# Kernel tuning notes

Measured on AMD Instinct MI355X. Metric: run time of the kernel, lower is better.

The kernel has to match this reference:

```python
import jax, jax.numpy as jnp
import numpy as np
from jax.scipy.special import logsumexp

TEMPERATURE = 0.1
EPS = 1e-8  # matches torch F.cosine_similarity eps


def setup_inputs() -> dict:
    key = jax.random.key(0)
    k1, k2 = jax.random.split(key)
    N, D, NUM_CLASSES = 8192, 256, 64
    embeddings = jax.random.normal(k1, (N, D), dtype=jnp.float32)
    target = jax.random.randint(k2, (N,), 0, NUM_CLASSES, dtype=jnp.int64)
    return {"embeddings": embeddings, "target": target}


def reference(embeddings, target):
    N = target.shape[0]
    # cosine similarity: normalize rows, then a single GEMM for all pairs
    norms = jnp.linalg.norm(embeddings, axis=-1, keepdims=True)
    e = embeddings / jnp.maximum(norms, EPS)
    sim = (e @ e.T) / TEMPERATURE  # [N, N]

    pos = target[:, None] == target[None, :]  # [N, N] bool, incl. diagonal
    diag = jnp.eye(N, dtype=bool)
    neg_inf = jnp.asarray(-jnp.inf, dtype=sim.dtype)

    # denominator: negatives only (positives masked to -inf)
    lse_neg = logsumexp(jnp.where(pos, neg_inf, sim), axis=1)
    # numerator: positives excluding self (diagonal masked to -inf)
    lse_pos = logsumexp(jnp.where(pos & ~diag, sim, neg_inf), axis=1)

    loss = lse_neg - lse_pos
    return loss.sum()
```

## Files before the change

kernel.cpp:

```cpp
#include <hip/hip_runtime.h>
#include <hip/hip_bf16.h>
#include <stdint.h>
#include <math.h>

#define NROWS 8192
#define DIM   256
#define RB    256
#define BI    128
#define JBLK  512
#define NBJS  4
#define NG    (NROWS/JBLK)
#define NIT   (NROWS/BI)

typedef __attribute__((ext_vector_type(4)))  int   int4v;
typedef __attribute__((ext_vector_type(8)))  int   int8v;
typedef __attribute__((ext_vector_type(16))) float floatx16;

typedef const __attribute__((address_space(1))) uint32_t gas_u32;
typedef __attribute__((address_space(3))) uint32_t las_u32;

#define SCALE_1_16 0x7B7B7B7B
#define L2E10      14.4269504088896f

__device__ __forceinline__ void gload_lds16(const void* g, void* l) {
    __builtin_amdgcn_global_load_lds((gas_u32*)(uintptr_t)g,
                                     (las_u32*)(uintptr_t)l, 16, 0, 0);
}

__global__ __launch_bounds__(256) void normalize_kernel(const float* __restrict__ emb,
                                                        uint32_t* __restrict__ e8,
                                                        float* __restrict__ out)
{
    if (blockIdx.x == 0 && threadIdx.x == 0) *out = 0.f;
    int row  = blockIdx.x * 4 + (threadIdx.x >> 6);
    int lane = threadIdx.x & 63;
    const float4* rowp = (const float4*)(emb + (size_t)row * DIM);
    float4 v = rowp[lane];
    float ss = v.x*v.x + v.y*v.y + v.z*v.z + v.w*v.w;
    #pragma unroll
    for (int off = 32; off > 0; off >>= 1)
        ss += __shfl_xor(ss, off, 64);
    float inv = 16.0f / fmaxf(sqrtf(ss), 1e-8f);
    int r = __builtin_amdgcn_cvt_pk_fp8_f32(v.x * inv, v.y * inv, 0, false);
    r     = __builtin_amdgcn_cvt_pk_fp8_f32(v.z * inv, v.w * inv, r, true);
    e8[(size_t)row * (DIM / 4) + lane] = (uint32_t)r;
}

template<bool DIAG>
__device__ __forceinline__ void epi(const floatx16 acc[2][2],
                                    const int* __restrict__ tgt,
                                    int jb, const int tiv[2], const int ic[2],
                                    float ps[2], float ts[2])
{
    #pragma unroll
    for (int jt = 0; jt < 2; ++jt) {
        #pragma unroll
        for (int rq = 0; rq < 4; ++rq) {
            const int jg_ = jb + jt * 32 + rq * 8;
            const int4v t4 = *(const int4v*)(tgt + jg_);
            #pragma unroll
            for (int it = 0; it < 2; ++it) {
                const int tivc = tiv[it];
                #pragma unroll
                for (int r2 = 0; r2 < 4; ++r2) {
                    float v = exp2f(fmaf(L2E10, acc[jt][it][rq * 4 + r2], -L2E10));
                    if (DIAG) {
                        if (jg_ + r2 == ic[it]) v = 0.f;
                    }
                    ts[it] += v;
                    ps[it] += (t4[r2] == tivc) ? v : 0.f;
                }
            }
        }
    }
}

__global__ __launch_bounds__(256, 2) void tile_kernel(const uint8_t* __restrict__ e8,
                                                      const int* __restrict__ tgt,
                                                      float* __restrict__ pps,
                                                      float* __restrict__ pts)
{
    __shared__ uint8_t buf[2][BI * RB];

    const int bi   = blockIdx.x;
    const int jg   = blockIdx.y;
    const int tid  = threadIdx.x;
    const int wave = tid >> 6;
    const int lane = tid & 63;
    const int col  = lane & 31;
    const int h    = lane >> 5;

    const int wr = (wave >> 1) * 64;
    const int wc = (wave & 1) * 64;

    int goff[8];
    #pragma unroll
    for (int t = 0; t < 8; ++t) {
        int s   = wave * 512 + t * 64 + lane;
        int row = s >> 4;
        int lc  = (s & 15) ^ (row & 15);
        goff[t] = row * RB + lc * 16;
    }

    const char* gB = (const char*)(e8 + (size_t)bi * BI * RB);
    const char* gA = (const char*)(e8 + (size_t)jg * JBLK * RB);

    #pragma unroll
    for (int t = 0; t < 8; ++t)
        gload_lds16(gA + goff[t], buf[0] + wave * 8192 + t * 1024);
    #pragma unroll
    for (int t = 0; t < 8; ++t)
        gload_lds16(gB + goff[t], buf[1] + wave * 8192 + t * 1024);
    __syncthreads();

    const int xm = col & 15;
    int poff[4][2];
    #pragma unroll
    for (int s = 0; s < 4; ++s)
        #pragma unroll
        for (int c = 0; c < 2; ++c)
            poff[s][c] = ((s * 4 + h * 2 + c) ^ xm) << 4;

    int8v bfr[2][4];
    #pragma unroll
    for (int it = 0; it < 2; ++it) {
        const uint8_t* pb = buf[1] + (wc + it * 32 + col) * RB;
        #pragma unroll
        for (int s = 0; s < 4; ++s) {
            int4v lo = *(const int4v*)(pb + poff[s][0]);
            int4v hi = *(const int4v*)(pb + poff[s][1]);
            bfr[it][s] = __builtin_shufflevector(lo, hi, 0, 1, 2, 3, 4, 5, 6, 7);
        }
    }
    __syncthreads();

    int tiv[2], ic[2];
    #pragma unroll
    for (int it = 0; it < 2; ++it) {
        ic[it]  = bi * BI + wc + it * 32 + col;
        tiv[it] = tgt[ic[it]];
    }

    float ps[2] = {0.f, 0.f};
    float ts[2] = {0.f, 0.f};

    const int dbi = bi - jg * 4;

    for (int bjs = 0; bjs < NBJS; ++bjs) {
        if (bjs < NBJS - 1) {
            const char* gAn = gA + (size_t)(bjs + 1) * BI * RB;
            #pragma unroll
            for (int t = 0; t < 8; ++t)
                gload_lds16(gAn + goff[t], buf[(bjs + 1) & 1] + wave * 8192 + t * 1024);
        }

        const uint8_t* ab = buf[bjs & 1];
        floatx16 acc[2][2];
        #pragma unroll
        for (int a = 0; a < 2; ++a)
            #pragma unroll
            for (int b = 0; b < 2; ++b)
                acc[a][b] = (floatx16){0.f,0.f,0.f,0.f,0.f,0.f,0.f,0.f,
                                       0.f,0.f,0.f,0.f,0.f,0.f,0.f,0.f};

        #pragma unroll
        for (int s = 0; s < 4; ++s) {
            int8v af[2];
            #pragma unroll
            for (int jt = 0; jt < 2; ++jt) {
                const uint8_t* pa = ab + (wr + jt * 32 + col) * RB;
                int4v lo = *(const int4v*)(pa + poff[s][0]);
                int4v hi = *(const int4v*)(pa + poff[s][1]);
                af[jt] = __builtin_shufflevector(lo, hi, 0, 1, 2, 3, 4, 5, 6, 7);
            }
            #pragma unroll
            for (int jt = 0; jt < 2; ++jt)
                #pragma unroll
                for (int it = 0; it < 2; ++it)
                    acc[jt][it] = __builtin_amdgcn_mfma_scale_f32_32x32x64_f8f6f4(
                        af[jt], bfr[it][s], acc[jt][it], 0, 0,
                        0, SCALE_1_16, 0, SCALE_1_16);
        }

        const int jb = jg * JBLK + bjs * BI + wr + h * 4;
        if (bjs == dbi)
            epi<true >(acc, tgt, jb, tiv, ic, ps, ts);
        else
            epi<false>(acc, tgt, jb, tiv, ic, ps, ts);

        if (bjs < NBJS - 1)
            __syncthreads();
    }

    #pragma unroll
    for (int it = 0; it < 2; ++it) {
        ps[it] += __shfl_xor(ps[it], 32, 64);
        ts[it] += __shfl_xor(ts[it], 32, 64);
    }
    if (h == 0) {
        const size_t base = (size_t)jg * NROWS;
        #pragma unroll
        for (int it = 0; it < 2; ++it) {
            pps[base + ic[it]] = ps[it];
            pts[base + ic[it]] = ts[it];
        }
    }
}

__global__ __launch_bounds__(256) void finalize_kernel(const float* __restrict__ pps,
                                                       const float* __restrict__ pts,
                                                       float* __restrict__ out)
{
    const int i = blockIdx.x * 256 + threadIdx.x;
    float sp = 0.f, st = 0.f;
    #pragma unroll
    for (int t = 0; t < NG; ++t) {
        sp += pps[(size_t)t * NROWS + i];
        st += pts[(size_t)t * NROWS + i];
    }
    float ns = st - sp;
    float loss = logf(ns) - logf(sp);
    #pragma unroll
    for (int off = 32; off > 0; off >>= 1)
        loss += __shfl_xor(loss, off, 64);
    __shared__ float w4[4];
    if ((threadIdx.x & 63) == 0) w4[threadIdx.x >> 6] = loss;
    __syncthreads();
    if (threadIdx.x == 0)
        atomicAdd(out, w4[0] + w4[1] + w4[2] + w4[3]);
}

extern "C" void kernel_launch(void* const* d_in, const int* in_sizes, int n_in,
                              void* d_out, int out_size, void* d_ws, size_t ws_size,
                              hipStream_t stream)
{
    (void)in_sizes; (void)n_in; (void)out_size; (void)ws_size;
    const float* emb = (const float*)d_in[0];
    const int*   tgt = (const int*)d_in[1];
    float*       out = (float*)d_out;

    uint32_t* e8  = (uint32_t*)d_ws;
    float*    pps = (float*)((char*)d_ws + (size_t)NROWS * RB);
    float*    pts = pps + (size_t)NG * NROWS;

    normalize_kernel<<<NROWS / 4, 256, 0, stream>>>(emb, e8, out);

    dim3 grid(NIT, NG);
    tile_kernel<<<grid, 256, 0, stream>>>((const uint8_t*)e8, tgt, pps, pts);

    finalize_kernel<<<NROWS / 256, 256, 0, stream>>>(pps, pts, out);
}
```

Measured before the change: 98.00 us.

## Retile similarity kernel to 128x64 sub-tiles with per-wave column ownership and higher occupancy

```diff
diff --git a/kernel.cpp b/kernel.cpp
--- a/kernel.cpp
+++ b/kernel.cpp
@@ -7,8 +7,9 @@
 #define DIM   256
 #define RB    256
 #define BI    128
-#define JBLK  512
-#define NBJS  4
+#define JSUB  64
+#define NBJS  8
+#define JBLK  (JSUB*NBJS)
 #define NG    (NROWS/JBLK)
 #define NIT   (NROWS/BI)
 
@@ -47,40 +48,36 @@
 }
 
 template<bool DIAG>
-__device__ __forceinline__ void epi(const floatx16 acc[2][2],
+__device__ __forceinline__ void epi(const floatx16 acc[2],
                                     const int* __restrict__ tgt,
-                                    int jb, const int tiv[2], const int ic[2],
-                                    float ps[2], float ts[2])
+                                    int jbs, int h, int ic0, int tiv0,
+                                    float& ps, float& ts)
 {
     #pragma unroll
     for (int jt = 0; jt < 2; ++jt) {
         #pragma unroll
         for (int rq = 0; rq < 4; ++rq) {
-            const int jg_ = jb + jt * 32 + rq * 8;
+            const int jg_ = jbs + jt * 32 + rq * 8 + h * 4;
             const int4v t4 = *(const int4v*)(tgt + jg_);
             #pragma unroll
-            for (int it = 0; it < 2; ++it) {
-                const int tivc = tiv[it];
-                #pragma unroll
-                for (int r2 = 0; r2 < 4; ++r2) {
-                    float v = exp2f(fmaf(L2E10, acc[jt][it][rq * 4 + r2], -L2E10));
-                    if (DIAG) {
-                        if (jg_ + r2 == ic[it]) v = 0.f;
-                    }
-                    ts[it] += v;
-                    ps[it] += (t4[r2] == tivc) ? v : 0.f;
+            for (int r2 = 0; r2 < 4; ++r2) {
+                float v = exp2f(fmaf(L2E10, acc[jt][rq * 4 + r2], -L2E10));
+                if (DIAG) {
+                    if (jg_ + r2 == ic0) v = 0.f;
                 }
+                ts += v;
+                ps += (t4[r2] == tiv0) ? v : 0.f;
             }
         }
     }
 }
 
-__global__ __launch_bounds__(256, 2) void tile_kernel(const uint8_t* __restrict__ e8,
+__global__ __launch_bounds__(256, 4) void tile_kernel(const uint8_t* __restrict__ e8,
                                                       const int* __restrict__ tgt,
                                                       float* __restrict__ pps,
                                                       float* __restrict__ pts)
 {
-    __shared__ uint8_t buf[2][BI * RB];
+    __shared__ uint8_t buf[2][JSUB * RB];
 
     const int bi   = blockIdx.x;
     const int jg   = blockIdx.y;
@@ -90,120 +87,89 @@
     const int col  = lane & 31;
     const int h    = lane >> 5;
 
-    const int wr = (wave >> 1) * 64;
-    const int wc = (wave & 1) * 64;
-
-    int goff[8];
-    #pragma unroll
-    for (int t = 0; t < 8; ++t) {
-        int s   = wave * 512 + t * 64 + lane;
+    const uint8_t* pb = e8 + (size_t)(bi * BI + wave * 32 + col) * RB + h * 32;
+    int8v bfr[4];
+    #pragma unroll
+    for (int s = 0; s < 4; ++s)
+        bfr[s] = *(const int8v*)(pb + s * 64);
+
+    int goffA[4];
+    #pragma unroll
+    for (int t = 0; t < 4; ++t) {
+        int s   = wave * 256 + t * 64 + lane;
         int row = s >> 4;
         int lc  = (s & 15) ^ (row & 15);
-        goff[t] = row * RB + lc * 16;
-    }
-
-    const char* gB = (const char*)(e8 + (size_t)bi * BI * RB);
+        goffA[t] = row * RB + lc * 16;
+    }
     const char* gA = (const char*)(e8 + (size_t)jg * JBLK * RB);
 
     #pragma unroll
-    for (int t = 0; t < 8; ++t)
-        gload_lds16(gA + goff[t], buf[0] + wave * 8192 + t * 1024);
-    #pragma unroll
-    for (int t = 0; t < 8; ++t)
-        gload_lds16(gB + goff[t], buf[1] + wave * 8192 + t * 1024);
+    for (int t = 0; t < 4; ++t)
+        gload_lds16(gA + goffA[t], buf[0] + wave * 4096 + t * 1024);
+
+    const int ic0  = bi * BI + wave * 32 + col;
+    const int tiv0 = tgt[ic0];
+
+    const int xm = col & 15;
+    int poff[4];
+    #pragma unroll
+    for (int s = 0; s < 4; ++s)
+        poff[s] = ((s * 4 + h * 2) ^ xm) << 4;
+
     __syncthreads();
 
-    const int xm = col & 15;
-    int poff[4][2];
-    #pragma unroll
-    for (int s = 0; s < 4; ++s)
-        #pragma unroll
-        for (int c = 0; c < 2; ++c)
-            poff[s][c] = ((s * 4 + h * 2 + c) ^ xm) << 4;
-
-    int8v bfr[2][4];
-    #pragma unroll
-    for (int it = 0; it < 2; ++it) {
-        const uint8_t* pb = buf[1] + (wc + it * 32 + col) * RB;
-        #pragma unroll
-        for (int s = 0; s < 4; ++s) {
-            int4v lo = *(const int4v*)(pb + poff[s][0]);
-            int4v hi = *(const int4v*)(pb + poff[s][1]);
-            bfr[it][s] = __builtin_shufflevector(lo, hi, 0, 1, 2, 3, 4, 5, 6, 7);
-        }
-    }
-    __syncthreads();
-
-    int tiv[2], ic[2];
-    #pragma unroll
-    for (int it = 0; it < 2; ++it) {
-        ic[it]  = bi * BI + wc + it * 32 + col;
-        tiv[it] = tgt[ic[it]];
-    }
-
-    float ps[2] = {0.f, 0.f};
-    float ts[2] = {0.f, 0.f};
-
-    const int dbi = bi - jg * 4;
-
+    float ps = 0.f, ts = 0.f;
+    const int dpair = bi - jg * 4;
+
+    #pragma unroll
     for (int bjs = 0; bjs < NBJS; ++bjs) {
         if (bjs < NBJS - 1) {
-            const char* gAn = gA + (size_t)(bjs + 1) * BI * RB;
-            #pragma unroll
-            for (int t = 0; t < 8; ++t)
-                gload_lds16(gAn + goff[t], buf[(bjs + 1) & 1] + wave * 8192 + t * 1024);
+            const char* gAn = gA + (size_t)(bjs + 1) * JSUB * RB;
+            #pragma unroll
+            for (int t = 0; t < 4; ++t)
+                gload_lds16(gAn + goffA[t], buf[(bjs + 1) & 1] + wave * 4096 + t * 1024);
         }
 
         const uint8_t* ab = buf[bjs & 1];
-        floatx16 acc[2][2];
+        floatx16 acc[2];
         #pragma unroll
-        for (int a = 0; a < 2; ++a)
-            #pragma unroll
-            for (int b = 0; b < 2; ++b)
-                acc[a][b] = (floatx16){0.f,0.f,0.f,0.f,0.f,0.f,0.f,0.f,
-                                       0.f,0.f,0.f,0.f,0.f,0.f,0.f,0.f};
+        for (int jt = 0; jt < 2; ++jt)
+            acc[jt] = (floatx16){0.f,0.f,0.f,0.f,0.f,0.f,0.f,0.f,
+                                 0.f,0.f,0.f,0.f,0.f,0.f,0.f,0.f};
 
         #pragma unroll
         for (int s = 0; s < 4; ++s) {
             int8v af[2];
             #pragma unroll
             for (int jt = 0; jt < 2; ++jt) {
-                const uint8_t* pa = ab + (wr + jt * 32 + col) * RB;
-                int4v lo = *(const int4v*)(pa + poff[s][0]);
-                int4v hi = *(const int4v*)(pa + poff[s][1]);
+                const uint8_t* pa = ab + (jt * 32 + col) * RB;
+                int4v lo = *(const int4v*)(pa + poff[s]);
+                int4v hi = *(const int4v*)(pa + (poff[s] ^ 16));
                 af[jt] = __builtin_shufflevector(lo, hi, 0, 1, 2, 3, 4, 5, 6, 7);
             }
             #pragma unroll
             for (int jt = 0; jt < 2; ++jt)
-                #pragma unroll
-                for (int it = 0; it < 2; ++it)
-                    acc[jt][it] = __builtin_amdgcn_mfma_scale_f32_32x32x64_f8f6f4(
-                        af[jt], bfr[it][s], acc[jt][it], 0, 0,
-                        0, SCALE_1_16, 0, SCALE_1_16);
+                acc[jt] = __builtin_amdgcn_mfma_scale_f32_32x32x64_f8f6f4(
+                    af[jt], bfr[s], acc[jt], 0, 0,
+                    0, SCALE_1_16, 0, SCALE_1_16);
         }
 
-        const int jb = jg * JBLK + bjs * BI + wr + h * 4;
-        if (bjs == dbi)
-            epi<true >(acc, tgt, jb, tiv, ic, ps, ts);
+        const int jbs = jg * JBLK + bjs * JSUB;
+        if ((bjs >> 1) == dpair)
+            epi<true >(acc, tgt, jbs, h, ic0, tiv0, ps, ts);
         else
-            epi<false>(acc, tgt, jb, tiv, ic, ps, ts);
+            epi<false>(acc, tgt, jbs, h, ic0, tiv0, ps, ts);
 
         if (bjs < NBJS - 1)
             __syncthreads();
     }
 
-    #pragma unroll
-    for (int it = 0; it < 2; ++it) {
-        ps[it] += __shfl_xor(ps[it], 32, 64);
-        ts[it] += __shfl_xor(ts[it], 32, 64);
-    }
+    ps += __shfl_xor(ps, 32, 64);
+    ts += __shfl_xor(ts, 32, 64);
     if (h == 0) {
         const size_t base = (size_t)jg * NROWS;
-        #pragma unroll
-        for (int it = 0; it < 2; ++it) {
-            pps[base + ic[it]] = ps[it];
-            pts[base + ic[it]] = ts[it];
-        }
+        pps[base + ic0] = ps;
+        pts[base + ic0] = ts;
     }
 }
 
```

Measured after the change: 102.3 us. 4.4% more time.
